# Optimization experiments

Measured on AMD Instinct MI355X. Metric: run time of the kernel, lower is better.

The kernel has to match this reference:

```python
import jax, jax.numpy as jnp
import numpy as np

N_NODES = 100000
N_EDGES = 800000
NODE_DIM = 128
EDGE_DIM = 32
MSG_DIM = 128
EPS = 1e-5


def layer_norm(x, g, b):
    mu = jnp.mean(x, axis=-1, keepdims=True)
    var = jnp.var(x, axis=-1, keepdims=True)
    return (x - mu) * jax.lax.rsqrt(var + EPS) * g + b


def he_normal(key, shape):
    # kaiming_normal_ with nonlinearity='relu': std = sqrt(2 / fan_in)
    fan_in = shape[1]
    return jax.random.normal(key, shape, dtype=jnp.float32) * np.sqrt(2.0 / fan_in)


def setup_inputs() -> dict:
    key = jax.random.key(0)
    ks = jax.random.split(key, 8)
    nodes = jax.random.normal(ks[0], (N_NODES, NODE_DIM), dtype=jnp.float32)
    edge_index = jax.random.randint(ks[1], (2, N_EDGES), 0, N_NODES, dtype=jnp.int64)
    edge_attr = jax.random.normal(ks[2], (N_EDGES, EDGE_DIM), dtype=jnp.float32)
    # torch Linear weights are [out, in]
    W_message = he_normal(ks[3], (MSG_DIM, NODE_DIM + EDGE_DIM))
    W_node = he_normal(ks[4], (NODE_DIM, NODE_DIM))
    W1 = he_normal(ks[5], (NODE_DIM, NODE_DIM + MSG_DIM))
    b1 = jnp.zeros((NODE_DIM,), dtype=jnp.float32)
    ln1_g = jnp.ones((NODE_DIM,), dtype=jnp.float32)
    ln1_b = jnp.zeros((NODE_DIM,), dtype=jnp.float32)
    W2 = he_normal(ks[6], (NODE_DIM, NODE_DIM))
    b2 = jnp.zeros((NODE_DIM,), dtype=jnp.float32)
    ln2_g = jnp.ones((NODE_DIM,), dtype=jnp.float32)
    ln2_b = jnp.zeros((NODE_DIM,), dtype=jnp.float32)
    ln_g = jnp.ones((NODE_DIM,), dtype=jnp.float32)
    ln_b = jnp.zeros((NODE_DIM,), dtype=jnp.float32)
    return {"nodes": nodes, "edge_index": edge_index, "edge_attr": edge_attr,
            "W_message": W_message, "W_node": W_node,
            "W1": W1, "b1": b1, "ln1_g": ln1_g, "ln1_b": ln1_b,
            "W2": W2, "b2": b2, "ln2_g": ln2_g, "ln2_b": ln2_b,
            "ln_g": ln_g, "ln_b": ln_b}


def reference(nodes, edge_index, edge_attr, W_message, W_node,
              W1, b1, ln1_g, ln1_b, W2, b2, ln2_g, ln2_b, ln_g, ln_b):
    senders, receivers = edge_index[0], edge_index[1]
    n_nodes = nodes.shape[0]
    # gather -> linear
    sender_features = nodes[senders]                                  # [E, node_dim]
    message_input = jnp.concatenate([sender_features, edge_attr], -1)  # [E, node_dim+edge_dim]
    messages = message_input @ W_message.T                            # [E, msg_dim]
    # scatter sum aggregation
    aggregated = jax.ops.segment_sum(messages, receivers, num_segments=n_nodes)
    # node MLP (two Linear+ReLU+LayerNorm blocks)
    node_input = jnp.concatenate([nodes, aggregated], -1)             # [N, node_dim+msg_dim]
    h = layer_norm(jax.nn.relu(node_input @ W1.T + b1), ln1_g, ln1_b)
    node_out = layer_norm(jax.nn.relu(h @ W2.T + b2), ln2_g, ln2_b)
    # residual + final LayerNorm
    return layer_norm(nodes @ W_node.T + node_out, ln_g, ln_b)
```

## Files before the change

### kernel.cpp

```cpp
#include <hip/hip_runtime.h>
#include <math.h>


#define THREADS 256
#define BM 64
#define BK 32
#define APB 40
#define BP 132

typedef __attribute__((ext_vector_type(8))) short bf16x8;
typedef __attribute__((ext_vector_type(4))) float f32x4;

struct GemmSmem {
  unsigned short As[BM][APB];
  unsigned short Bs[128][APB];
};
struct EpiSmem {
  float Cs[BM][BP];
  float psum[BM][4];
  float psq[BM][4];
  float mu[BM];
  float rs[BM];
};

union BF8 { bf16x8 v; ushort4 q[2]; };

__device__ __forceinline__ unsigned short f2bf(float x) {
  union { float f; unsigned u; } c; c.f = x;
  unsigned u = c.u;
  u += 0x7fffu + ((u >> 16) & 1u);
  return (unsigned short)(u >> 16);
}
__device__ __forceinline__ float bf2f(unsigned h) {
  union { unsigned u; float f; } c; c.u = h << 16; return c.f;
}
__device__ __forceinline__ ushort4 cvt4(float4 v) {
  ushort4 p; p.x = f2bf(v.x); p.y = f2bf(v.y); p.z = f2bf(v.z); p.w = f2bf(v.w);
  return p;
}

__global__ __launch_bounds__(256) void prep_kernel(
    const float* __restrict__ W1, const float* __restrict__ Wm,
    const float* __restrict__ W2, const float* __restrict__ Wn,
    const float* __restrict__ nodes, const int* __restrict__ eidx,
    unsigned short* __restrict__ Wcat, unsigned short* __restrict__ W2b,
    unsigned short* __restrict__ Wnb, unsigned short* __restrict__ nodes_bf,
    int* __restrict__ counts, int Nn, int E, int nconv) {
  const int b = blockIdx.x, tid = threadIdx.x;
  if (b < 128) {
    for (int t = tid; t < 288; t += 256) {
      float v;
      if (t < 128) {
        v = W1[(size_t)b * 256 + t];
      } else {
        int u = t - 128;
        float s = 0.f;
#pragma unroll 8
        for (int k = 0; k < 128; ++k)
          s += W1[(size_t)b * 256 + 128 + k] * Wm[(size_t)k * 160 + u];
        v = s;
      }
      Wcat[(size_t)b * 288 + t] = f2bf(v);
    }
  } else if (b < 144) {
    int idx = (b - 128) * 1024 + tid * 4;
    *(ushort4*)&W2b[idx] = cvt4(*(const float4*)&W2[idx]);
  } else if (b < 160) {
    int idx = (b - 144) * 1024 + tid * 4;
    *(ushort4*)&Wnb[idx] = cvt4(*(const float4*)&Wn[idx]);
  } else if (b < 160 + nconv) {
    int idx = ((b - 160) * 256 + tid) * 4;
    if (idx < Nn * 128)
      *(ushort4*)&nodes_bf[idx] = cvt4(*(const float4*)&nodes[idx]);
  } else {
    int i = (b - 160 - nconv) * 256 + tid;
    if (i < E) atomicAdd(&counts[eidx[E + i]], 1);
  }
}

__global__ __launch_bounds__(256) void scan1_kernel(const int* __restrict__ counts,
                                                    int* __restrict__ bsum, int Nn) {
  __shared__ int red[256];
  const int tid = threadIdx.x;
  int base = blockIdx.x * 2048 + tid * 8;
  int s = 0;
#pragma unroll
  for (int i = 0; i < 8; ++i) {
    int idx = base + i;
    if (idx < Nn) s += counts[idx];
  }
  red[tid] = s;
  __syncthreads();
#pragma unroll
  for (int off = 128; off; off >>= 1) {
    if (tid < off) red[tid] += red[tid + off];
    __syncthreads();
  }
  if (tid == 0) bsum[blockIdx.x] = red[0];
}

__global__ __launch_bounds__(256) void scan2_kernel(const int* __restrict__ bsum,
                                                    int* __restrict__ boff, int NB) {
  __shared__ int arr[256];
  const int tid = threadIdx.x;
  int v = (tid < NB) ? bsum[tid] : 0;
  arr[tid] = v;
  __syncthreads();
  for (int off = 1; off < 256; off <<= 1) {
    int t2 = (tid >= off) ? arr[tid - off] : 0;
    __syncthreads();
    arr[tid] += t2;
    __syncthreads();
  }
  if (tid < NB) boff[tid] = arr[tid] - v;
}

__global__ __launch_bounds__(256) void scan3_kernel(const int* __restrict__ counts,
                                                    const int* __restrict__ boff,
                                                    int* __restrict__ row_ptr,
                                                    int* __restrict__ cursor, int Nn) {
  __shared__ int arr[256];
  const int tid = threadIdx.x;
  int base = blockIdx.x * 2048 + tid * 8;
  int c[8];
  int s = 0;
#pragma unroll
  for (int i = 0; i < 8; ++i) {
    int idx = base + i;
    c[i] = (idx < Nn) ? counts[idx] : 0;
    s += c[i];
  }
  arr[tid] = s;
  __syncthreads();
  for (int off = 1; off < 256; off <<= 1) {
    int t2 = (tid >= off) ? arr[tid - off] : 0;
    __syncthreads();
    arr[tid] += t2;
    __syncthreads();
  }
  int run = arr[tid] - s + boff[blockIdx.x];
#pragma unroll
  for (int i = 0; i < 8; ++i) {
    int idx = base + i;
    if (idx < Nn) {
      row_ptr[idx] = run;
      cursor[idx] = run;
    }
    run += c[i];
  }
}

__global__ __launch_bounds__(256) void build_kernel(const int* __restrict__ eidx,
                                                    int* __restrict__ cursor,
                                                    int2* __restrict__ ps, int E) {
  int i = blockIdx.x * 256 + threadIdx.x;
  if (i < E) {
    int r = eidx[E + i];
    int pos = atomicAdd(&cursor[r], 1);
    ps[pos] = make_int2(eidx[i], i);
  }
}

__global__ __launch_bounds__(256) void aggsum_kernel(
    const unsigned short* __restrict__ nodes_bf, const float* __restrict__ eattr,
    const int* __restrict__ row_ptr, const int* __restrict__ rend,
    const int2* __restrict__ ps, unsigned short* __restrict__ S, int Nn) {
  const int wid = blockIdx.x * 4 + (threadIdx.x >> 6);
  if (wid >= Nn) return;
  const int lane = threadIdx.x & 63;
  const int start = row_ptr[wid];
  const int end = rend[wid];
  const int deg = end - start;
  const int dmax = deg < 64 ? deg : 64;

  int sv = 0, pv = 0;
  if (lane < deg) {
    int2 sp = ps[start + lane];
    sv = sp.x;
    pv = sp.y;
  }

  const unsigned* nodes32 = (const unsigned*)nodes_bf;
  const int rsub = lane >> 5;
  const int col = lane & 31;
  float s0 = 0.f, s1 = 0.f, se = 0.f;

  for (int t0 = 0; t0 < dmax; t0 += 8) {
    unsigned a[8];
    float ev[4];
#pragma unroll
    for (int k = 0; k < 8; ++k) {
      int tt = t0 + k;
      if (tt > dmax - 1) tt = dmax - 1;
      int idx = __builtin_amdgcn_readlane(sv, tt);
      a[k] = nodes32[(size_t)idx * 64 + lane];
    }
#pragma unroll
    for (int k = 0; k < 4; ++k) {
      int tt = t0 + 2 * k + rsub;
      if (tt > dmax - 1) tt = dmax - 1;
      int p = __shfl(pv, tt);
      ev[k] = eattr[(size_t)p * 32 + col];
    }
#pragma unroll
    for (int k = 0; k < 8; ++k) {
      if (t0 + k < dmax) {
        s0 += bf2f(a[k] & 0xffffu);
        s1 += bf2f(a[k] >> 16);
      }
    }
#pragma unroll
    for (int k = 0; k < 4; ++k) {
      se += (t0 + 2 * k + rsub < dmax) ? ev[k] : 0.f;
    }
  }

  for (int j = start + 64; j < end; ++j) {
    int2 sp = ps[j];
    unsigned a = nodes32[(size_t)sp.x * 64 + lane];
    s0 += bf2f(a & 0xffffu);
    s1 += bf2f(a >> 16);
    if (rsub == 0) se += eattr[(size_t)sp.y * 32 + col];
  }

  se += __shfl_xor(se, 32);

  unsigned pack = (unsigned)f2bf(s0) | ((unsigned)f2bf(s1) << 16);
  ((unsigned*)S)[(size_t)wid * 80 + lane] = pack;

  float lo = __shfl(se, 2 * (lane & 15));
  float hi = __shfl(se, 2 * (lane & 15) + 1);
  if (lane < 16) {
    unsigned p2 = (unsigned)f2bf(lo) | ((unsigned)f2bf(hi) << 16);
    ((unsigned*)S)[(size_t)wid * 80 + 64 + lane] = p2;
  }
}

__device__ __forceinline__ void gemm_chunk(const GemmSmem& sm, int tid,
                                           f32x4 acc[2][4]) {
  const int lane = tid & 63;
  const int quad = lane >> 4;
  const int lm = lane & 15;
  const int wid = tid >> 6;
  const int wy = wid >> 1, wx = wid & 1;

  bf16x8 af[2], bf[4];
#pragma unroll
  for (int mt = 0; mt < 2; ++mt)
    af[mt] = *(const bf16x8*)&sm.As[32 * wy + 16 * mt + lm][quad * 8];
#pragma unroll
  for (int nt = 0; nt < 4; ++nt)
    bf[nt] = *(const bf16x8*)&sm.Bs[64 * wx + 16 * nt + lm][quad * 8];
#pragma unroll
  for (int mt = 0; mt < 2; ++mt)
#pragma unroll
    for (int nt = 0; nt < 4; ++nt)
      acc[mt][nt] = __builtin_amdgcn_mfma_f32_16x16x32_bf16(
          af[mt], bf[nt], acc[mt][nt], 0, 0, 0);
}

__device__ __forceinline__ void stage_A(const unsigned short* __restrict__ A,
                                        int row0, int Nn, int kc, int tid, BF8& ta) {
  int r = tid >> 2, u = tid & 3;
  int row = row0 + r;
  if (row >= Nn) row = Nn - 1;
  ta.v = *(const bf16x8*)&A[(size_t)row * 128 + kc + 8 * u];
}
__device__ __forceinline__ void stage_A_cat(const unsigned short* __restrict__ A0,
                                            const unsigned short* __restrict__ A1,
                                            int row0, int Nn, int kc, int tid,
                                            BF8& ta) {
  int r = tid >> 2, u = tid & 3;
  int k = kc + 8 * u;
  int row = row0 + r;
  if (row >= Nn) row = Nn - 1;
  if (kc >= 128)
    ta.v = *(const bf16x8*)&A1[(size_t)row * 160 + (k - 128)];
  else
    ta.v = *(const bf16x8*)&A0[(size_t)row * 128 + k];
}
__device__ __forceinline__ void stage_B(const unsigned short* __restrict__ W,
                                        int ldw, int kc, int tid, BF8 tb[2]) {
#pragma unroll
  for (int c = 0; c < 2; ++c) {
    int f = tid + 256 * c;
    int n = f >> 2, u = f & 3;
    tb[c].v = *(const bf16x8*)&W[(size_t)n * ldw + kc + 8 * u];
  }
}
__device__ __forceinline__ void write_A(GemmSmem& g, int tid, const BF8& ta) {
  int r = tid >> 2, u = tid & 3;
  *(ushort4*)&g.As[r][8 * u] = ta.q[0];
  *(ushort4*)&g.As[r][8 * u + 4] = ta.q[1];
}
__device__ __forceinline__ void write_B(GemmSmem& g, int tid, const BF8 tb[2]) {
#pragma unroll
  for (int c = 0; c < 2; ++c) {
    int f = tid + 256 * c;
    int n = f >> 2, u = f & 3;
    *(ushort4*)&g.Bs[n][8 * u] = tb[c].q[0];
    *(ushort4*)&g.Bs[n][8 * u + 4] = tb[c].q[1];
  }
}

__device__ __forceinline__ void gemm_k128(const unsigned short* __restrict__ A,
                                          const unsigned short* __restrict__ W,
                                          int row0, int Nn, GemmSmem& g, int tid,
                                          f32x4 acc[2][4]) {
  BF8 ta, tb[2], na, nb[2];
  stage_A(A, row0, Nn, 0, tid, ta);
  stage_B(W, 128, 0, tid, tb);
  for (int kc = 0; kc < 128; kc += BK) {
    write_A(g, tid, ta);
    write_B(g, tid, tb);
    __syncthreads();
    if (kc + BK < 128) {
      stage_A(A, row0, Nn, kc + BK, tid, na);
      stage_B(W, 128, kc + BK, tid, nb);
    }
    gemm_chunk(g, tid, acc);
    __syncthreads();
    ta = na;
    tb[0] = nb[0];
    tb[1] = nb[1];
  }
}

__device__ __forceinline__ void gemm_k128_lds(const EpiSmem& e,
                                              const unsigned short* __restrict__ W,
                                              GemmSmem& g, int tid,
                                              f32x4 acc[2][4]) {
  BF8 tb[2], nb[2];
  stage_B(W, 128, 0, tid, tb);
  for (int kc = 0; kc < 128; kc += BK) {
    {
      int r = tid >> 2, u = tid & 3;
      float4 lo = *(const float4*)&e.Cs[r][kc + 8 * u];
      float4 hi = *(const float4*)&e.Cs[r][kc + 8 * u + 4];
      *(ushort4*)&g.As[r][8 * u] = cvt4(lo);
      *(ushort4*)&g.As[r][8 * u + 4] = cvt4(hi);
    }
    write_B(g, tid, tb);
    __syncthreads();
    if (kc + BK < 128) stage_B(W, 128, kc + BK, tid, nb);
    gemm_chunk(g, tid, acc);
    __syncthreads();
    tb[0] = nb[0];
    tb[1] = nb[1];
  }
}

__device__ __forceinline__ void ln_stats(EpiSmem& e, int tid) {
  {
    int q = tid & 3, r = tid >> 2;
    float s = 0.f, s2 = 0.f;
#pragma unroll 8
    for (int j = q * 32; j < q * 32 + 32; ++j) {
      float x = e.Cs[r][j];
      s += x;
      s2 += x * x;
    }
    e.psum[r][q] = s;
    e.psq[r][q] = s2;
  }
  __syncthreads();
  if (tid < BM) {
    float S_ = 0.f, S2 = 0.f;
#pragma unroll
    for (int q = 0; q < 4; ++q) {
      S_ += e.psum[tid][q];
      S2 += e.psq[tid][q];
    }
    float m = S_ * (1.f / 128.f);
    float var = S2 * (1.f / 128.f) - m * m;
    e.mu[tid] = m;
    e.rs[tid] = rsqrtf(var + 1e-5f);
  }
  __syncthreads();
}

__global__ __launch_bounds__(THREADS, 3) void node_fused_kernel(
    const unsigned short* __restrict__ A0, const unsigned short* __restrict__ A1,
    const unsigned short* __restrict__ Wcat, const float* __restrict__ b1,
    const float* __restrict__ g1, const float* __restrict__ bl1,
    const unsigned short* __restrict__ W2b, const unsigned short* __restrict__ Wnb,
    const float* __restrict__ b2, const float* __restrict__ g2,
    const float* __restrict__ bl2, const float* __restrict__ gf,
    const float* __restrict__ blf, float* __restrict__ out, int Nn) {
  __shared__ GemmSmem g;
  __shared__ EpiSmem e;
  const int tid = threadIdx.x;
  const int row0 = blockIdx.x * BM;
  const int lane = tid & 63;
  const int quad = lane >> 4;
  const int lm = lane & 15;
  const int wid = tid >> 6;
  const int wy = wid >> 1, wx = wid & 1;

  f32x4 acc[2][4];
#pragma unroll
  for (int mt = 0; mt < 2; ++mt)
#pragma unroll
    for (int nt = 0; nt < 4; ++nt) acc[mt][nt] = (f32x4)0.f;

  {
    BF8 ta, tb[2], na, nb[2];
    stage_A_cat(A0, A1, row0, Nn, 0, tid, ta);
    stage_B(Wcat, 288, 0, tid, tb);
    for (int kc = 0; kc < 288; kc += BK) {
      write_A(g, tid, ta);
      write_B(g, tid, tb);
      __syncthreads();
      if (kc + BK < 288) {
        stage_A_cat(A0, A1, row0, Nn, kc + BK, tid, na);
        stage_B(Wcat, 288, kc + BK, tid, nb);
      }
      gemm_chunk(g, tid, acc);
      __syncthreads();
      ta = na;
      tb[0] = nb[0];
      tb[1] = nb[1];
    }
  }

  {
    float bval[4];
#pragma unroll
    for (int nt = 0; nt < 4; ++nt) bval[nt] = b1[64 * wx + 16 * nt + lm];
#pragma unroll
    for (int mt = 0; mt < 2; ++mt)
#pragma unroll
      for (int i = 0; i < 4; ++i) {
        int r = 32 * wy + 16 * mt + quad * 4 + i;
#pragma unroll
        for (int nt = 0; nt < 4; ++nt) {
          int col = 64 * wx + 16 * nt + lm;
          e.Cs[r][col] = fmaxf(acc[mt][nt][i] + bval[nt], 0.f);
        }
      }
  }
  __syncthreads();
  ln_stats(e, tid);
#pragma unroll 4
  for (int s = 0; s < 32; ++s) {
    int flat = tid + THREADS * s;
    int r = flat >> 7, j = flat & 127;
    float x = e.Cs[r][j];
    e.Cs[r][j] = (x - e.mu[r]) * e.rs[r] * g1[j] + bl1[j];
  }
  __syncthreads();

#pragma unroll
  for (int mt = 0; mt < 2; ++mt)
#pragma unroll
    for (int nt = 0; nt < 4; ++nt) acc[mt][nt] = (f32x4)0.f;

  gemm_k128_lds(e, W2b, g, tid, acc);

  {
    float bval[4];
#pragma unroll
    for (int nt = 0; nt < 4; ++nt) bval[nt] = b2[64 * wx + 16 * nt + lm];
#pragma unroll
    for (int mt = 0; mt < 2; ++mt)
#pragma unroll
      for (int i = 0; i < 4; ++i) {
        int r = 32 * wy + 16 * mt + quad * 4 + i;
#pragma unroll
        for (int nt = 0; nt < 4; ++nt) {
          int col = 64 * wx + 16 * nt + lm;
          e.Cs[r][col] = fmaxf(acc[mt][nt][i] + bval[nt], 0.f);
        }
      }
  }
  __syncthreads();
  ln_stats(e, tid);
#pragma unroll 4
  for (int s = 0; s < 32; ++s) {
    int flat = tid + THREADS * s;
    int r = flat >> 7, j = flat & 127;
    float x = e.Cs[r][j];
    e.Cs[r][j] = (x - e.mu[r]) * e.rs[r] * g2[j] + bl2[j];
  }
  __syncthreads();

#pragma unroll
  for (int mt = 0; mt < 2; ++mt)
#pragma unroll
    for (int nt = 0; nt < 4; ++nt) acc[mt][nt] = (f32x4)0.f;

  gemm_k128(A0, Wnb, row0, Nn, g, tid, acc);

#pragma unroll
  for (int mt = 0; mt < 2; ++mt)
#pragma unroll
    for (int i = 0; i < 4; ++i) {
      int r = 32 * wy + 16 * mt + quad * 4 + i;
#pragma unroll
      for (int nt = 0; nt < 4; ++nt) {
        int col = 64 * wx + 16 * nt + lm;
        e.Cs[r][col] = acc[mt][nt][i] + e.Cs[r][col];
      }
    }
  __syncthreads();
  ln_stats(e, tid);

#pragma unroll 4
  for (int s = 0; s < 32; ++s) {
    int flat = tid + THREADS * s;
    int r = flat >> 7, j = flat & 127;
    int row = row0 + r;
    if (row < Nn) {
      float x = e.Cs[r][j];
      out[(size_t)row * 128 + j] =
          (x - e.mu[r]) * e.rs[r] * gf[j] + blf[j];
    }
  }
}

extern "C" void kernel_launch(void* const* d_in, const int* in_sizes, int n_in,
                              void* d_out, int out_size, void* d_ws, size_t ws_size,
                              hipStream_t stream) {
  const float* nodes = (const float*)d_in[0];
  const int* eidx    = (const int*)d_in[1];
  const float* eattr = (const float*)d_in[2];
  const float* Wm    = (const float*)d_in[3];
  const float* Wn    = (const float*)d_in[4];
  const float* W1    = (const float*)d_in[5];
  const float* b1    = (const float*)d_in[6];
  const float* g1    = (const float*)d_in[7];
  const float* bl1   = (const float*)d_in[8];
  const float* W2    = (const float*)d_in[9];
  const float* b2    = (const float*)d_in[10];
  const float* g2    = (const float*)d_in[11];
  const float* bl2   = (const float*)d_in[12];
  const float* gf    = (const float*)d_in[13];
  const float* blf   = (const float*)d_in[14];
  float* out = (float*)d_out;

  const int Nn = in_sizes[0] / 128;
  const int E  = in_sizes[2] / 32;

  int* counts  = (int*)d_ws;
  int* row_ptr = counts + Nn;
  int* cursor  = row_ptr + Nn;
  int* bsum    = cursor + Nn;
  int* boff    = bsum + 256;
  int2* ps     = (int2*)(boff + 256);
  unsigned short* Wcat     = (unsigned short*)((int*)ps + 2 * (size_t)E);
  unsigned short* W2b      = Wcat + 128 * 288;
  unsigned short* Wnb      = W2b + 128 * 128;
  unsigned short* nodes_bf = Wnb + 128 * 128;
  unsigned short* S_bf     = nodes_bf + (size_t)Nn * 128;

  hipMemsetAsync(counts, 0, (size_t)Nn * sizeof(int), stream);

  const int nconv = (Nn * 32 + 255) / 256;
  const int nhist = (E + 255) / 256;
  const int NB = (Nn + 2047) / 2048;
  const int ngrid = (Nn + BM - 1) / BM;

  prep_kernel<<<160 + nconv + nhist, 256, 0, stream>>>(
      W1, Wm, W2, Wn, nodes, eidx, Wcat, W2b, Wnb, nodes_bf, counts, Nn, E, nconv);
  scan1_kernel<<<NB, 256, 0, stream>>>(counts, bsum, Nn);
  scan2_kernel<<<1, 256, 0, stream>>>(bsum, boff, NB);
  scan3_kernel<<<NB, 256, 0, stream>>>(counts, boff, row_ptr, cursor, Nn);
  build_kernel<<<nhist, 256, 0, stream>>>(eidx, cursor, ps, E);
  aggsum_kernel<<<(Nn + 3) / 4, 256, 0, stream>>>(nodes_bf, eattr, row_ptr, cursor,
                                                  ps, S_bf, Nn);
  node_fused_kernel<<<ngrid, THREADS, 0, stream>>>(
      nodes_bf, S_bf, Wcat, b1, g1, bl1, W2b, Wnb, b2, g2, bl2, gf, blf, out, Nn);
}
```

Before: 420.8 us.

## Make node kernel persistent and widen LDS stores, interleave LN stats reads

Turns the fused node kernel into a grid-stride persistent kernel with at most 768 blocks, each looping over 64-row tiles instead of one block per tile. It also merges paired 8-byte LDS stores into single 16-byte stores, and changes the LayerNorm partial-sum loop to a strided column pattern meant to reduce LDS bank conflicts. The persistent grid is meant to cut block launch and tail overhead. The cost is reliance on occupancy of about three blocks per CU to hide latency, and a possible load imbalance when the number of tiles does not divide evenly across blocks.

```diff
diff --git a/kernel.cpp b/kernel.cpp
--- a/kernel.cpp
+++ b/kernel.cpp
@@ -7,6 +7,7 @@
 #define BK 32
 #define APB 40
 #define BP 132
+#define PGRID 768
 
 typedef __attribute__((ext_vector_type(8))) short bf16x8;
 typedef __attribute__((ext_vector_type(4))) float f32x4;
@@ -290,16 +291,14 @@
 }
 __device__ __forceinline__ void write_A(GemmSmem& g, int tid, const BF8& ta) {
   int r = tid >> 2, u = tid & 3;
-  *(ushort4*)&g.As[r][8 * u] = ta.q[0];
-  *(ushort4*)&g.As[r][8 * u + 4] = ta.q[1];
+  *(bf16x8*)&g.As[r][8 * u] = ta.v;
 }
 __device__ __forceinline__ void write_B(GemmSmem& g, int tid, const BF8 tb[2]) {
 #pragma unroll
   for (int c = 0; c < 2; ++c) {
     int f = tid + 256 * c;
     int n = f >> 2, u = f & 3;
-    *(ushort4*)&g.Bs[n][8 * u] = tb[c].q[0];
-    *(ushort4*)&g.Bs[n][8 * u + 4] = tb[c].q[1];
+    *(bf16x8*)&g.Bs[n][8 * u] = tb[c].v;
   }
 }
 
@@ -335,10 +334,10 @@
   for (int kc = 0; kc < 128; kc += BK) {
     {
       int r = tid >> 2, u = tid & 3;
-      float4 lo = *(const float4*)&e.Cs[r][kc + 8 * u];
-      float4 hi = *(const float4*)&e.Cs[r][kc + 8 * u + 4];
-      *(ushort4*)&g.As[r][8 * u] = cvt4(lo);
-      *(ushort4*)&g.As[r][8 * u + 4] = cvt4(hi);
+      BF8 t;
+      t.q[0] = cvt4(*(const float4*)&e.Cs[r][kc + 8 * u]);
+      t.q[1] = cvt4(*(const float4*)&e.Cs[r][kc + 8 * u + 4]);
+      *(bf16x8*)&g.As[r][8 * u] = t.v;
     }
     write_B(g, tid, tb);
     __syncthreads();
@@ -355,8 +354,8 @@
     int q = tid & 3, r = tid >> 2;
     float s = 0.f, s2 = 0.f;
 #pragma unroll 8
-    for (int j = q * 32; j < q * 32 + 32; ++j) {
-      float x = e.Cs[r][j];
+    for (int j = 0; j < 32; ++j) {
+      float x = e.Cs[r][q + 4 * j];
       s += x;
       s2 += x * x;
     }
@@ -386,47 +385,113 @@
     const unsigned short* __restrict__ W2b, const unsigned short* __restrict__ Wnb,
     const float* __restrict__ b2, const float* __restrict__ g2,
     const float* __restrict__ bl2, const float* __restrict__ gf,
-    const float* __restrict__ blf, float* __restrict__ out, int Nn) {
+    const float* __restrict__ blf, float* __restrict__ out, int Nn, int ntiles) {
   __shared__ GemmSmem g;
   __shared__ EpiSmem e;
   const int tid = threadIdx.x;
-  const int row0 = blockIdx.x * BM;
   const int lane = tid & 63;
   const int quad = lane >> 4;
   const int lm = lane & 15;
   const int wid = tid >> 6;
   const int wy = wid >> 1, wx = wid & 1;
 
-  f32x4 acc[2][4];
-#pragma unroll
-  for (int mt = 0; mt < 2; ++mt)
-#pragma unroll
-    for (int nt = 0; nt < 4; ++nt) acc[mt][nt] = (f32x4)0.f;
-
-  {
-    BF8 ta, tb[2], na, nb[2];
-    stage_A_cat(A0, A1, row0, Nn, 0, tid, ta);
-    stage_B(Wcat, 288, 0, tid, tb);
-    for (int kc = 0; kc < 288; kc += BK) {
-      write_A(g, tid, ta);
-      write_B(g, tid, tb);
-      __syncthreads();
-      if (kc + BK < 288) {
-        stage_A_cat(A0, A1, row0, Nn, kc + BK, tid, na);
-        stage_B(Wcat, 288, kc + BK, tid, nb);
+  for (int tile = blockIdx.x; tile < ntiles; tile += gridDim.x) {
+    const int row0 = tile * BM;
+
+    f32x4 acc[2][4];
+#pragma unroll
+    for (int mt = 0; mt < 2; ++mt)
+#pragma unroll
+      for (int nt = 0; nt < 4; ++nt) acc[mt][nt] = (f32x4)0.f;
+
+    {
+      BF8 ta, tb[2], na, nb[2];
+      stage_A_cat(A0, A1, row0, Nn, 0, tid, ta);
+      stage_B(Wcat, 288, 0, tid, tb);
+      for (int kc = 0; kc < 288; kc += BK) {
+        write_A(g, tid, ta);
+        write_B(g, tid, tb);
+        __syncthreads();
+        if (kc + BK < 288) {
+          stage_A_cat(A0, A1, row0, Nn, kc + BK, tid, na);
+          stage_B(Wcat, 288, kc + BK, tid, nb);
+        }
+        gemm_chunk(g, tid, acc);
+        __syncthreads();
+        ta = na;
+        tb[0] = nb[0];
+        tb[1] = nb[1];
       }
-      gemm_chunk(g, tid, acc);
-      __syncthreads();
-      ta = na;
-      tb[0] = nb[0];
-      tb[1] = nb[1];
-    }
-  }
-
-  {
-    float bval[4];
-#pragma unroll
-    for (int nt = 0; nt < 4; ++nt) bval[nt] = b1[64 * wx + 16 * nt + lm];
+    }
+
+    {
+      float bval[4];
+#pragma unroll
+      for (int nt = 0; nt < 4; ++nt) bval[nt] = b1[64 * wx + 16 * nt + lm];
+#pragma unroll
+      for (int mt = 0; mt < 2; ++mt)
+#pragma unroll
+        for (int i = 0; i < 4; ++i) {
+          int r = 32 * wy + 16 * mt + quad * 4 + i;
+#pragma unroll
+          for (int nt = 0; nt < 4; ++nt) {
+            int col = 64 * wx + 16 * nt + lm;
+            e.Cs[r][col] = fmaxf(acc[mt][nt][i] + bval[nt], 0.f);
+          }
+        }
+    }
+    __syncthreads();
+    ln_stats(e, tid);
+#pragma unroll 4
+    for (int s = 0; s < 32; ++s) {
+      int flat = tid + THREADS * s;
+      int r = flat >> 7, j = flat & 127;
+      float x = e.Cs[r][j];
+      e.Cs[r][j] = (x - e.mu[r]) * e.rs[r] * g1[j] + bl1[j];
+    }
+    __syncthreads();
+
+#pragma unroll
+    for (int mt = 0; mt < 2; ++mt)
+#pragma unroll
+      for (int nt = 0; nt < 4; ++nt) acc[mt][nt] = (f32x4)0.f;
+
+    gemm_k128_lds(e, W2b, g, tid, acc);
+
+    {
+      float bval[4];
+#pragma unroll
+      for (int nt = 0; nt < 4; ++nt) bval[nt] = b2[64 * wx + 16 * nt + lm];
+#pragma unroll
+      for (int mt = 0; mt < 2; ++mt)
+#pragma unroll
+        for (int i = 0; i < 4; ++i) {
+          int r = 32 * wy + 16 * mt + quad * 4 + i;
+#pragma unroll
+          for (int nt = 0; nt < 4; ++nt) {
+            int col = 64 * wx + 16 * nt + lm;
+            e.Cs[r][col] = fmaxf(acc[mt][nt][i] + bval[nt], 0.f);
+          }
+        }
+    }
+    __syncthreads();
+    ln_stats(e, tid);
+#pragma unroll 4
+    for (int s = 0; s < 32; ++s) {
+      int flat = tid + THREADS * s;
+      int r = flat >> 7, j = flat & 127;
+      float x = e.Cs[r][j];
+      e.Cs[r][j] = (x - e.mu[r]) * e.rs[r] * g2[j] + bl2[j];
+    }
+    __syncthreads();
+
+#pragma unroll
+    for (int mt = 0; mt < 2; ++mt)
+#pragma unroll
+      for (int nt = 0; nt < 4; ++nt) acc[mt][nt] = (f32x4)0.f;
+
+    gemm_k128(A0, Wnb, row0, Nn, g, tid, acc);
+
 #pragma unroll
     for (int mt = 0; mt < 2; ++mt)
 #pragma unroll
@@ -435,85 +500,22 @@
 #pragma unroll
         for (int nt = 0; nt < 4; ++nt) {
           int col = 64 * wx + 16 * nt + lm;
-          e.Cs[r][col] = fmaxf(acc[mt][nt][i] + bval[nt], 0.f);
+          e.Cs[r][col] = acc[mt][nt][i] + e.Cs[r][col];
         }
       }
-  }
-  __syncthreads();
-  ln_stats(e, tid);
+    __syncthreads();
+    ln_stats(e, tid);
+
 #pragma unroll 4
-  for (int s = 0; s < 32; ++s) {
-    int flat = tid + THREADS * s;
-    int r = flat >> 7, j = flat & 127;
-    float x = e.Cs[r][j];
-    e.Cs[r][j] = (x - e.mu[r]) * e.rs[r] * g1[j] + bl1[j];
-  }
-  __syncthreads();
-
-#pragma unroll
-  for (int mt = 0; mt < 2; ++mt)
-#pragma unroll
-    for (int nt = 0; nt < 4; ++nt) acc[mt][nt] = (f32x4)0.f;
-
-  gemm_k128_lds(e, W2b, g, tid, acc);
-
-  {
-    float bval[4];
-#pragma unroll
-    for (int nt = 0; nt < 4; ++nt) bval[nt] = b2[64 * wx + 16 * nt + lm];
-#pragma unroll
-    for (int mt = 0; mt < 2; ++mt)
-#pragma unroll
-      for (int i = 0; i < 4; ++i) {
-        int r = 32 * wy + 16 * mt + quad * 4 + i;
-#pragma unroll
-        for (int nt = 0; nt < 4; ++nt) {
-          int col = 64 * wx + 16 * nt + lm;
-          e.Cs[r][col] = fmaxf(acc[mt][nt][i] + bval[nt], 0.f);
-        }
+    for (int s = 0; s < 32; ++s) {
+      int flat = tid + THREADS * s;
+      int r = flat >> 7, j = flat & 127;
+      int row = row0 + r;
+      if (row < Nn) {
+        float x = e.Cs[r][j];
+        out[(size_t)row * 128 + j] =
+            (x - e.mu[r]) * e.rs[r] * gf[j] + blf[j];
       }
-  }
-  __syncthreads();
-  ln_stats(e, tid);
-#pragma unroll 4
-  for (int s = 0; s < 32; ++s) {
-    int flat = tid + THREADS * s;
-    int r = flat >> 7, j = flat & 127;
-    float x = e.Cs[r][j];
-    e.Cs[r][j] = (x - e.mu[r]) * e.rs[r] * g2[j] + bl2[j];
-  }
-  __syncthreads();
-
-#pragma unroll
-  for (int mt = 0; mt < 2; ++mt)
-#pragma unroll
-    for (int nt = 0; nt < 4; ++nt) acc[mt][nt] = (f32x4)0.f;
-
-  gemm_k128(A0, Wnb, row0, Nn, g, tid, acc);
-
-#pragma unroll
-  for (int mt = 0; mt < 2; ++mt)
-#pragma unroll
-    for (int i = 0; i < 4; ++i) {
-      int r = 32 * wy + 16 * mt + quad * 4 + i;
-#pragma unroll
-      for (int nt = 0; nt < 4; ++nt) {
-        int col = 64 * wx + 16 * nt + lm;
-        e.Cs[r][col] = acc[mt][nt][i] + e.Cs[r][col];
-      }
-    }
-  __syncthreads();
-  ln_stats(e, tid);
-
-#pragma unroll 4
-  for (int s = 0; s < 32; ++s) {
-    int flat = tid + THREADS * s;
-    int r = flat >> 7, j = flat & 127;
-    int row = row0 + r;
-    if (row < Nn) {
-      float x = e.Cs[r][j];
-      out[(size_t)row * 128 + j] =
-          (x - e.mu[r]) * e.rs[r] * gf[j] + blf[j];
     }
   }
 }
@@ -558,7 +560,8 @@
   const int nconv = (Nn * 32 + 255) / 256;
   const int nhist = (E + 255) / 256;
   const int NB = (Nn + 2047) / 2048;
-  const int ngrid = (Nn + BM - 1) / BM;
+  const int ntiles = (Nn + BM - 1) / BM;
+  const int pgrid = ntiles < PGRID ? ntiles : PGRID;
 
   prep_kernel<<<160 + nconv + nhist, 256, 0, stream>>>(
       W1, Wm, W2, Wn, nodes, eidx, Wcat, W2b, Wnb, nodes_bf, counts, Nn, E, nconv);
@@ -568,6 +571,7 @@
   build_kernel<<<nhist, 256, 0, stream>>>(eidx, cursor, ps, E);
   aggsum_kernel<<<(Nn + 3) / 4, 256, 0, stream>>>(nodes_bf, eattr, row_ptr, cursor,
                                                   ps, S_bf, Nn);
-  node_fused_kernel<<<ngrid, THREADS, 0, stream>>>(
-      nodes_bf, S_bf, Wcat, b1, g1, bl1, W2b, Wnb, b2, g2, bl2, gf, blf, out, Nn);
-}
+  node_fused_kernel<<<pgrid, THREADS, 0, stream>>>(
+      nodes_bf, S_bf, Wcat, b1, g1, bl1, W2b, Wnb, b2, g2, bl2, gf, blf, out, Nn,
+      ntiles);
+}
```

Result: slower. 453.5 us (+7.8%).
